# Optimization experiments

Hardware: AMD Instinct MI355X
Metric: run time of the kernel (lower is better)

The kernel has to match this reference:

```python
import jax, jax.numpy as jnp
import numpy as np

DIM = 1024
NUM_HEADS = 16
HEAD_DIM = DIM // NUM_HEADS
THETA = 10000.0


def apply_rope(x):
    # x: [B, S, H, D]; Llama-style interleaved rotary pairs.
    S, D = x.shape[1], x.shape[3]
    half = D // 2
    inv_freq = THETA ** (-jnp.arange(half, dtype=jnp.float32) * 2.0 / D)  # [D/2]
    angles = jnp.arange(S, dtype=jnp.float32)[:, None] * inv_freq[None, :]  # [S, D/2]
    cos = jnp.cos(angles)[None, :, None, :]  # [1,S,1,D/2]
    sin = jnp.sin(angles)[None, :, None, :]
    x_even = x[..., 0::2]
    x_odd = x[..., 1::2]
    out_even = x_even * cos - x_odd * sin
    out_odd = x_even * sin + x_odd * cos
    out = jnp.stack([out_even, out_odd], axis=-1).reshape(x.shape)
    return out.astype(x.dtype)


def setup_inputs() -> dict:
    key = jax.random.key(0)
    ks = jax.random.split(key, 5)
    B, S = 2, 2048
    x = jax.random.normal(ks[0], (B, S, DIM), dtype=jnp.float32)
    scale = 1.0 / np.sqrt(DIM)
    Wq = jax.random.normal(ks[1], (DIM, DIM), dtype=jnp.float32) * scale
    Wk = jax.random.normal(ks[2], (DIM, DIM), dtype=jnp.float32) * scale
    Wv = jax.random.normal(ks[3], (DIM, DIM), dtype=jnp.float32) * scale
    Wo = jax.random.normal(ks[4], (DIM, DIM), dtype=jnp.float32) * scale
    return {"x": x, "Wq": Wq, "Wk": Wk, "Wv": Wv, "Wo": Wo}


def reference(x, Wq, Wk, Wv, Wo):
    B, S, _ = x.shape
    # torch Linear: y = x @ W^T
    q = (x @ Wq.T).reshape(B, S, NUM_HEADS, HEAD_DIM)
    k = (x @ Wk.T).reshape(B, S, NUM_HEADS, HEAD_DIM)
    v = (x @ Wv.T).reshape(B, S, NUM_HEADS, HEAD_DIM)
    q = apply_rope(q)
    k = apply_rope(k)
    # causal SDPA, scale = 1/sqrt(head_dim)
    scale = 1.0 / np.sqrt(HEAD_DIM).astype(np.float32)
    scores = jnp.einsum("bqhd,bkhd->bhqk", q, k) * scale  # [B,H,S,S]
    causal = jnp.tril(jnp.ones((S, S), dtype=bool))
    scores = jnp.where(causal[None, None], scores, jnp.finfo(scores.dtype).min)
    attn = jax.nn.softmax(scores, axis=-1)
    y = jnp.einsum("bhqk,bkhd->bqhd", attn, v).reshape(B, S, DIM)
    return y @ Wo.T
```

## Files before the change

kernel.cpp:

```cpp
#include <hip/hip_runtime.h>
#include <hip/hip_bf16.h>

typedef __attribute__((ext_vector_type(8))) __bf16 bf16x8;
typedef __attribute__((ext_vector_type(4))) __bf16 bf16x4;
typedef __attribute__((ext_vector_type(4))) float f32x4;

#define DIM 1024
#define SLEN 2048
#define NH 16
#define HD 64

__device__ __forceinline__ f32x4 MFMA(bf16x8 a, bf16x8 b, f32x4 c) {
    return __builtin_amdgcn_mfma_f32_16x16x32_bf16(a, b, c, 0, 0, 0);
}

__global__ __launch_bounds__(256) void cvt_bf16(const float* __restrict__ in,
                                                __bf16* __restrict__ out, int n) {
    int i = (blockIdx.x * blockDim.x + threadIdx.x) * 8;
    if (i >= n) return;
    f32x4 a = *reinterpret_cast<const f32x4*>(in + i);
    f32x4 b = *reinterpret_cast<const f32x4*>(in + i + 4);
    bf16x8 o;
#pragma unroll
    for (int j = 0; j < 4; ++j) { o[j] = (__bf16)a[j]; o[j + 4] = (__bf16)b[j]; }
    *reinterpret_cast<bf16x8*>(out + i) = o;
}

__global__ __launch_bounds__(256) void cvt_w4(const float* __restrict__ w0,
                                              const float* __restrict__ w1,
                                              const float* __restrict__ w2,
                                              const float* __restrict__ w3,
                                              __bf16* __restrict__ o0,
                                              __bf16* __restrict__ o1,
                                              __bf16* __restrict__ o2,
                                              __bf16* __restrict__ o3) {
    int s = blockIdx.y;
    const float* in = s == 0 ? w0 : s == 1 ? w1 : s == 2 ? w2 : w3;
    __bf16* out = s == 0 ? o0 : s == 1 ? o1 : s == 2 ? o2 : o3;
    int i = (blockIdx.x * blockDim.x + threadIdx.x) * 8;
    f32x4 a = *reinterpret_cast<const f32x4*>(in + i);
    f32x4 b = *reinterpret_cast<const f32x4*>(in + i + 4);
    bf16x8 o;
#pragma unroll
    for (int j = 0; j < 4; ++j) { o[j] = (__bf16)a[j]; o[j + 4] = (__bf16)b[j]; }
    *reinterpret_cast<bf16x8*>(out + i) = o;
}

__global__ __launch_bounds__(256) void rope2(__bf16* __restrict__ q,
                                             __bf16* __restrict__ k) {
    __bf16* t = blockIdx.y == 0 ? q : k;
    const float scale = blockIdx.y == 0 ? 0.18033688011112042f : 1.0f;
    int idx = blockIdx.x * blockDim.x + threadIdx.x;
    int row = idx >> 9;
    int p = idx & 511;
    int head = p >> 5;
    int j = p & 31;
    int s = row & (SLEN - 1);
    float inv = expf(-0.28782313662425574f * (float)j);
    float angle = (float)s * inv;
    float sn, cs;
    sincosf(angle, &sn, &cs);
    size_t base = (size_t)row * DIM + head * HD + 2 * j;
    float e = (float)t[base], o = (float)t[base + 1];
    t[base] = (__bf16)((e * cs - o * sn) * scale);
    t[base + 1] = (__bf16)((e * sn + o * cs) * scale);
}

__global__ __launch_bounds__(256) void gemm_qkv(const __bf16* __restrict__ X,
                                                const __bf16* __restrict__ Wq,
                                                const __bf16* __restrict__ Wk,
                                                const __bf16* __restrict__ Wv,
                                                __bf16* __restrict__ Qo,
                                                __bf16* __restrict__ Ko,
                                                __bf16* __restrict__ Vt) {
    __shared__ alignas(16) __bf16 Alds[128 * 64];
    __shared__ alignas(16) __bf16 Blds[128 * 64];
    const int tid = threadIdx.x;
    const int lane = tid & 63;
    const int w = tid >> 6;
    const int wr = w >> 1, wc = w & 1;
    const int l15 = lane & 15, lhi = lane >> 4;
    const int l7 = l15 & 7;
    const int m0 = blockIdx.y * 128;
    const int n0g = blockIdx.x * 128;
    const int seg = n0g >> 10;
    const int n0 = n0g & 1023;
    const __bf16* __restrict__ B = seg == 0 ? Wq : seg == 1 ? Wk : Wv;
    const int K = 1024, N = 1024;

    const int lrow = lane >> 3;
    const int scol = ((lane & 7) ^ lrow) * 8;

    f32x4 acc[4][4] = {};

    for (int kt = 0; kt < K; kt += 64) {
#pragma unroll
        for (int c = 0; c < 4; ++c) {
            int r0 = c * 32 + w * 8;
            const __bf16* sa = &X[(size_t)(m0 + r0 + lrow) * K + kt + scol];
            const __bf16* sb = &B[(size_t)(n0 + r0 + lrow) * K + kt + scol];
            __builtin_amdgcn_global_load_lds((const __attribute__((address_space(1))) void*)sa,
                                             (__attribute__((address_space(3))) void*)&Alds[r0 * 64],
                                             16, 0, 0);
            __builtin_amdgcn_global_load_lds((const __attribute__((address_space(1))) void*)sb,
                                             (__attribute__((address_space(3))) void*)&Blds[r0 * 64],
                                             16, 0, 0);
        }
        __syncthreads();
#pragma unroll
        for (int kk = 0; kk < 2; ++kk) {
            bf16x8 af[4], bfr[4];
#pragma unroll
            for (int i = 0; i < 4; ++i) {
                af[i] = *(const bf16x8*)&Alds[(wr * 64 + i * 16 + l15) * 64 + 8 * ((kk * 4 + lhi) ^ l7)];
                bfr[i] = *(const bf16x8*)&Blds[(wc * 64 + i * 16 + l15) * 64 + 8 * ((kk * 4 + lhi) ^ l7)];
            }
            __builtin_amdgcn_s_setprio(1);
#pragma unroll
            for (int i = 0; i < 4; ++i)
#pragma unroll
                for (int j = 0; j < 4; ++j)
                    acc[i][j] = MFMA(af[i], bfr[j], acc[i][j]);
            __builtin_amdgcn_s_setprio(0);
        }
        __syncthreads();
    }
    if (seg < 2) {
        __bf16* __restrict__ O = seg == 0 ? Qo : Ko;
#pragma unroll
        for (int i = 0; i < 4; ++i)
#pragma unroll
            for (int j = 0; j < 4; ++j)
#pragma unroll
                for (int r = 0; r < 4; ++r) {
                    int row = m0 + wr * 64 + i * 16 + lhi * 4 + r;
                    int col = n0 + wc * 64 + j * 16 + l15;
                    O[(size_t)row * N + col] = (__bf16)acc[i][j][r];
                }
    } else {
#pragma unroll
        for (int i = 0; i < 4; ++i)
#pragma unroll
            for (int j = 0; j < 4; ++j) {
                int row = m0 + wr * 64 + i * 16 + lhi * 4;
                int col = n0 + wc * 64 + j * 16 + l15;
                int bb = row >> 11, s = row & 2047;
                int hh = col >> 6, d = col & 63;
                bf16x4 pk;
#pragma unroll
                for (int r = 0; r < 4; ++r) pk[r] = (__bf16)acc[i][j][r];
                *(bf16x4*)&Vt[((size_t)(bb * 16 + hh) * 64 + d) * SLEN + s] = pk;
            }
    }
}

__global__ __launch_bounds__(256) void gemm_o(const __bf16* __restrict__ A,
                                              const __bf16* __restrict__ B,
                                              float* __restrict__ C) {
    __shared__ alignas(16) __bf16 Alds[64 * 64];
    __shared__ alignas(16) __bf16 Blds[128 * 64];
    const int tid = threadIdx.x;
    const int lane = tid & 63;
    const int w = tid >> 6;
    const int wr = w >> 1, wc = w & 1;
    const int l15 = lane & 15, lhi = lane >> 4;
    const int l7 = l15 & 7;
    const int m0 = blockIdx.y * 64;
    const int n0 = blockIdx.x * 128;
    const int K = 1024, N = 1024;

    const int lrow = lane >> 3;
    const int scol = ((lane & 7) ^ lrow) * 8;

    f32x4 acc[2][4] = {};

    for (int kt = 0; kt < K; kt += 64) {
#pragma unroll
        for (int c = 0; c < 2; ++c) {
            int r0 = c * 32 + w * 8;
            const __bf16* sa = &A[(size_t)(m0 + r0 + lrow) * K + kt + scol];
            __builtin_amdgcn_global_load_lds((const __attribute__((address_space(1))) void*)sa,
                                             (__attribute__((address_space(3))) void*)&Alds[r0 * 64],
                                             16, 0, 0);
        }
#pragma unroll
        for (int c = 0; c < 4; ++c) {
            int r0 = c * 32 + w * 8;
            const __bf16* sb = &B[(size_t)(n0 + r0 + lrow) * K + kt + scol];
            __builtin_amdgcn_global_load_lds((const __attribute__((address_space(1))) void*)sb,
                                             (__attribute__((address_space(3))) void*)&Blds[r0 * 64],
                                             16, 0, 0);
        }
        __syncthreads();
#pragma unroll
        for (int kk = 0; kk < 2; ++kk) {
            bf16x8 af[2], bfr[4];
#pragma unroll
            for (int i = 0; i < 2; ++i)
                af[i] = *(const bf16x8*)&Alds[(wr * 32 + i * 16 + l15) * 64 + 8 * ((kk * 4 + lhi) ^ l7)];
#pragma unroll
            for (int j = 0; j < 4; ++j)
                bfr[j] = *(const bf16x8*)&Blds[(wc * 64 + j * 16 + l15) * 64 + 8 * ((kk * 4 + lhi) ^ l7)];
            __builtin_amdgcn_s_setprio(1);
#pragma unroll
            for (int i = 0; i < 2; ++i)
#pragma unroll
                for (int j = 0; j < 4; ++j)
                    acc[i][j] = MFMA(af[i], bfr[j], acc[i][j]);
            __builtin_amdgcn_s_setprio(0);
        }
        __syncthreads();
    }
#pragma unroll
    for (int i = 0; i < 2; ++i)
#pragma unroll
        for (int j = 0; j < 4; ++j)
#pragma unroll
            for (int r = 0; r < 4; ++r) {
                int row = m0 + wr * 32 + i * 16 + lhi * 4 + r;
                int col = n0 + wc * 64 + j * 16 + l15;
                C[(size_t)row * N + col] = acc[i][j][r];
            }
}

__global__ __launch_bounds__(256) void attn_kernel(const __bf16* __restrict__ Q,
                                                   const __bf16* __restrict__ K,
                                                   const __bf16* __restrict__ Vt,
                                                   __bf16* __restrict__ Y) {
    __shared__ __bf16 Klds[2][64 * 64];
    __shared__ __bf16 Vlds[2][64 * 64];
    __shared__ __bf16 Plds[4][16][68];

    const int tid = threadIdx.x;
    const int lane = tid & 63;
    const int w = tid >> 6;
    const int l15 = lane & 15, lhi = lane >> 4;
    const int l7 = l15 & 7;

    const int id = blockIdx.x;
    const int x = id & 7, j = id >> 3;
    const int qt = 31 - (j >> 2);
    const int bh = 4 * x + (j & 3);
    const int b = bh >> 4, h = bh & 15;

    const int srow = (lane >> 3);
    const int scs = (lane & 7) ^ srow;
    const __bf16* Kbase = K + (size_t)b * SLEN * DIM + h * HD;
    const __bf16* Vbase = Vt + (size_t)bh * 64 * SLEN;

    auto stage = [&](int buf, int kt) {
#pragma unroll
        for (int i = 0; i < 2; ++i) {
            int r0 = i * 32 + 8 * w + srow;
            const __bf16* sk = Kbase + (size_t)(kt * 64 + r0) * DIM + scs * 8;
            const __bf16* sv = Vbase + (size_t)r0 * SLEN + kt * 64 + scs * 8;
            __builtin_amdgcn_global_load_lds((const __attribute__((address_space(1))) void*)sk,
                                             (__attribute__((address_space(3))) void*)&Klds[buf][r0 * 64],
                                             16, 0, 0);
            __builtin_amdgcn_global_load_lds((const __attribute__((address_space(1))) void*)sv,
                                             (__attribute__((address_space(3))) void*)&Vlds[buf][r0 * 64],
                                             16, 0, 0);
        }
    };

    const int q0 = qt * 64;
    const int qrow_g = q0 + w * 16 + l15;
    const size_t qbase = (size_t)(b * SLEN + qrow_g) * DIM + h * HD;
    const bf16x8 qf0 = *(const bf16x8*)&Q[qbase + lhi * 8];
    const bf16x8 qf1 = *(const bf16x8*)&Q[qbase + 32 + lhi * 8];

    float m = -1e30f, lsum = 0.f;
    f32x4 acc[4] = {};

    const int nkt = qt + 1;
    stage(0, 0);
    for (int kt = 0; kt < nkt; ++kt) {
        const int cur = kt & 1;
        __syncthreads();
        if (kt + 1 < nkt) stage(cur ^ 1, kt + 1);

        f32x4 sT[4];
        __builtin_amdgcn_s_setprio(1);
#pragma unroll
        for (int nb = 0; nb < 4; ++nb) {
            const int krow = (nb * 16 + l15) * 64;
            bf16x8 k0 = *(const bf16x8*)&Klds[cur][krow + 8 * ((0 + lhi) ^ l7)];
            bf16x8 k1 = *(const bf16x8*)&Klds[cur][krow + 8 * ((4 + lhi) ^ l7)];
            f32x4 a = {};
            a = MFMA(k0, qf0, a);
            a = MFMA(k1, qf1, a);
            sT[nb] = a;
        }
        __builtin_amdgcn_s_setprio(0);
        if (kt == qt) {
#pragma unroll
            for (int nb = 0; nb < 4; ++nb)
#pragma unroll
                for (int r = 0; r < 4; ++r)
                    if (nb * 16 + lhi * 4 + r > w * 16 + l15) sT[nb][r] = -1e30f;
        }
        float mx = -1e30f;
#pragma unroll
        for (int nb = 0; nb < 4; ++nb)
#pragma unroll
            for (int r = 0; r < 4; ++r) mx = fmaxf(mx, sT[nb][r]);
        mx = fmaxf(mx, __shfl_xor(mx, 16));
        mx = fmaxf(mx, __shfl_xor(mx, 32));
        if (!__all(mx <= m + 8.0f)) {
            const float mnew = fmaxf(m, mx);
            const float corr = exp2f(m - mnew);
            m = mnew;
            lsum *= corr;
#pragma unroll
            for (int nd = 0; nd < 4; ++nd)
#pragma unroll
                for (int r = 0; r < 4; ++r) acc[nd][r] *= corr;
        }
        float rs = 0.f;
#pragma unroll
        for (int nb = 0; nb < 4; ++nb) {
            bf16x4 pk;
#pragma unroll
            for (int r = 0; r < 4; ++r) {
                float pv = exp2f(sT[nb][r] - m);
                rs += pv;
                pk[r] = (__bf16)pv;
            }
            *(bf16x4*)&Plds[w][l15][nb * 16 + lhi * 4] = pk;
        }
        rs += __shfl_xor(rs, 16);
        rs += __shfl_xor(rs, 32);
        lsum += rs;

        __builtin_amdgcn_s_setprio(1);
#pragma unroll
        for (int kk = 0; kk < 2; ++kk) {
            const bf16x8 pf = *(const bf16x8*)&Plds[w][l15][kk * 32 + lhi * 8];
#pragma unroll
            for (int nd = 0; nd < 4; ++nd) {
                const int vrow = (nd * 16 + l15) * 64;
                bf16x8 vf = *(const bf16x8*)&Vlds[cur][vrow + 8 * ((kk * 4 + lhi) ^ l7)];
                acc[nd] = MFMA(vf, pf, acc[nd]);
            }
        }
        __builtin_amdgcn_s_setprio(0);
    }
    const float inv = 1.0f / lsum;
#pragma unroll
    for (int nd = 0; nd < 4; ++nd) {
        bf16x4 o;
#pragma unroll
        for (int r = 0; r < 4; ++r) o[r] = (__bf16)(acc[nd][r] * inv);
        *(bf16x4*)&Y[(size_t)(b * SLEN + qrow_g) * DIM + h * HD + nd * 16 + lhi * 4] = o;
    }
}

extern "C" void kernel_launch(void* const* d_in, const int* in_sizes, int n_in,
                              void* d_out, int out_size, void* d_ws, size_t ws_size,
                              hipStream_t stream) {
    const float* x = (const float*)d_in[0];
    const float* Wq = (const float*)d_in[1];
    const float* Wk = (const float*)d_in[2];
    const float* Wv = (const float*)d_in[3];
    const float* Wo = (const float*)d_in[4];
    float* out = (float*)d_out;

    const size_t XN = (size_t)4096 * 1024;
    const size_t WN = (size_t)1024 * 1024;

    __bf16* xb = (__bf16*)d_ws;
    __bf16* qb = xb + XN;
    __bf16* kb = qb + XN;
    __bf16* vtb = kb + XN;
    __bf16* wqb = vtb + XN;
    __bf16* wkb = wqb + WN;
    __bf16* wvb = wkb + WN;
    __bf16* wob = wvb + WN;
    __bf16* yb = xb;

    cvt_bf16<<<XN / 8 / 256, 256, 0, stream>>>(x, xb, (int)XN);
    dim3 gw(WN / 8 / 256, 4);
    cvt_w4<<<gw, 256, 0, stream>>>(Wq, Wk, Wv, Wo, wqb, wkb, wvb, wob);

    dim3 gq(24, 32);
    gemm_qkv<<<gq, 256, 0, stream>>>(xb, wqb, wkb, wvb, qb, kb, vtb);

    int pairs = 4096 * (DIM / 2);
    dim3 gr(pairs / 256, 2);
    rope2<<<gr, 256, 0, stream>>>(qb, kb);

    attn_kernel<<<1024, 256, 0, stream>>>(qb, kb, vtb, yb);

    dim3 go(8, 64);
    gemm_o<<<go, 256, 0, stream>>>(yb, wob, out);
}
```

Baseline: 118.7 us.

## Fuse RoPE into QKV GEMM epilogue and compute softmax row sums via MFMA

Removes the separate rope2 kernel and applies the rotary embedding (plus the Q scale) inside the QKV GEMM epilogue, using a lane shuffle to fetch the paired even/odd element and fast __sincosf. In attention, the per-row softmax denominator is accumulated with an extra MFMA against a vector of ones instead of scalar adds and cross-lane shuffles. The P tile in LDS loses its padding and uses an XOR swizzle instead, and the row max uses a flatter reduction tree. This saves one kernel launch and a full read/write pass over Q and K, at the cost of lower-precision sincos and summing the denominator from bf16-rounded probabilities.

```diff
diff --git a/kernel.cpp b/kernel.cpp
--- a/kernel.cpp
+++ b/kernel.cpp
@@ -44,26 +44,6 @@
 #pragma unroll
     for (int j = 0; j < 4; ++j) { o[j] = (__bf16)a[j]; o[j + 4] = (__bf16)b[j]; }
     *reinterpret_cast<bf16x8*>(out + i) = o;
-}
-
-__global__ __launch_bounds__(256) void rope2(__bf16* __restrict__ q,
-                                             __bf16* __restrict__ k) {
-    __bf16* t = blockIdx.y == 0 ? q : k;
-    const float scale = blockIdx.y == 0 ? 0.18033688011112042f : 1.0f;
-    int idx = blockIdx.x * blockDim.x + threadIdx.x;
-    int row = idx >> 9;
-    int p = idx & 511;
-    int head = p >> 5;
-    int j = p & 31;
-    int s = row & (SLEN - 1);
-    float inv = expf(-0.28782313662425574f * (float)j);
-    float angle = (float)s * inv;
-    float sn, cs;
-    sincosf(angle, &sn, &cs);
-    size_t base = (size_t)row * DIM + head * HD + 2 * j;
-    float e = (float)t[base], o = (float)t[base + 1];
-    t[base] = (__bf16)((e * cs - o * sn) * scale);
-    t[base + 1] = (__bf16)((e * sn + o * cs) * scale);
 }
 
 __global__ __launch_bounds__(256) void gemm_qkv(const __bf16* __restrict__ X,
@@ -127,16 +107,27 @@
     }
     if (seg < 2) {
         __bf16* __restrict__ O = seg == 0 ? Qo : Ko;
-#pragma unroll
-        for (int i = 0; i < 4; ++i)
-#pragma unroll
-            for (int j = 0; j < 4; ++j)
+        const float qscale = seg == 0 ? 0.18033688011112042f : 1.0f;
+#pragma unroll
+        for (int j = 0; j < 4; ++j) {
+            const int col = n0 + wc * 64 + j * 16 + l15;
+            const int jp = (col & 63) >> 1;
+            const bool codd = col & 1;
+            const float invf = expf(-0.28782313662425574f * (float)jp);
+#pragma unroll
+            for (int i = 0; i < 4; ++i)
 #pragma unroll
                 for (int r = 0; r < 4; ++r) {
                     int row = m0 + wr * 64 + i * 16 + lhi * 4 + r;
-                    int col = n0 + wc * 64 + j * 16 + l15;
-                    O[(size_t)row * N + col] = (__bf16)acc[i][j][r];
+                    int s = row & (SLEN - 1);
+                    float sn, cs;
+                    __sincosf((float)s * invf, &sn, &cs);
+                    float own = acc[i][j][r];
+                    float oth = __shfl_xor(own, 1);
+                    float res = codd ? (oth * sn + own * cs) : (own * cs - oth * sn);
+                    O[(size_t)row * N + col] = (__bf16)(res * qscale);
                 }
+        }
     } else {
 #pragma unroll
         for (int i = 0; i < 4; ++i)
@@ -229,7 +220,7 @@
                                                    __bf16* __restrict__ Y) {
     __shared__ __bf16 Klds[2][64 * 64];
     __shared__ __bf16 Vlds[2][64 * 64];
-    __shared__ __bf16 Plds[4][16][68];
+    __shared__ __bf16 Plds[4][16][64];
 
     const int tid = threadIdx.x;
     const int lane = tid & 63;
@@ -269,8 +260,13 @@
     const bf16x8 qf0 = *(const bf16x8*)&Q[qbase + lhi * 8];
     const bf16x8 qf1 = *(const bf16x8*)&Q[qbase + 32 + lhi * 8];
 
-    float m = -1e30f, lsum = 0.f;
+    bf16x8 ones;
+#pragma unroll
+    for (int t = 0; t < 8; ++t) ones[t] = (__bf16)1.0f;
+
+    float m = -1e30f;
     f32x4 acc[4] = {};
+    f32x4 accL = {};
 
     const int nkt = qt + 1;
     stage(0, 0);
@@ -299,43 +295,45 @@
                 for (int r = 0; r < 4; ++r)
                     if (nb * 16 + lhi * 4 + r > w * 16 + l15) sT[nb][r] = -1e30f;
         }
-        float mx = -1e30f;
-#pragma unroll
-        for (int nb = 0; nb < 4; ++nb)
-#pragma unroll
-            for (int r = 0; r < 4; ++r) mx = fmaxf(mx, sT[nb][r]);
+        float t0 = fmaxf(fmaxf(sT[0][0], sT[0][1]), sT[0][2]);
+        float t1 = fmaxf(fmaxf(sT[0][3], sT[1][0]), sT[1][1]);
+        float t2 = fmaxf(fmaxf(sT[1][2], sT[1][3]), sT[2][0]);
+        float t3 = fmaxf(fmaxf(sT[2][1], sT[2][2]), sT[2][3]);
+        float t4 = fmaxf(fmaxf(sT[3][0], sT[3][1]), sT[3][2]);
+        float mx = fmaxf(fmaxf(fmaxf(t0, t1), fmaxf(t2, t3)), fmaxf(t4, sT[3][3]));
         mx = fmaxf(mx, __shfl_xor(mx, 16));
         mx = fmaxf(mx, __shfl_xor(mx, 32));
         if (!__all(mx <= m + 8.0f)) {
             const float mnew = fmaxf(m, mx);
             const float corr = exp2f(m - mnew);
             m = mnew;
-            lsum *= corr;
 #pragma unroll
             for (int nd = 0; nd < 4; ++nd)
 #pragma unroll
                 for (int r = 0; r < 4; ++r) acc[nd][r] *= corr;
-        }
-        float rs = 0.f;
+#pragma unroll
+            for (int r = 0; r < 4; ++r) accL[r] *= corr;
+        }
 #pragma unroll
         for (int nb = 0; nb < 4; ++nb) {
             bf16x4 pk;
 #pragma unroll
-            for (int r = 0; r < 4; ++r) {
-                float pv = exp2f(sT[nb][r] - m);
-                rs += pv;
-                pk[r] = (__bf16)pv;
-            }
-            *(bf16x4*)&Plds[w][l15][nb * 16 + lhi * 4] = pk;
-        }
-        rs += __shfl_xor(rs, 16);
-        rs += __shfl_xor(rs, 32);
-        lsum += rs;
+            for (int r = 0; r < 4; ++r) pk[r] = (__bf16)exp2f(sT[nb][r] - m);
+            const int cw = (nb * 4 + lhi) ^ l15;
+            *(bf16x4*)&Plds[w][l15][cw * 4] = pk;
+        }
 
         __builtin_amdgcn_s_setprio(1);
 #pragma unroll
         for (int kk = 0; kk < 2; ++kk) {
-            const bf16x8 pf = *(const bf16x8*)&Plds[w][l15][kk * 32 + lhi * 8];
+            const int c0 = (kk * 8 + lhi * 2) ^ l15;
+            const int c1 = c0 ^ 1;
+            bf16x4 plo = *(const bf16x4*)&Plds[w][l15][c0 * 4];
+            bf16x4 phi = *(const bf16x4*)&Plds[w][l15][c1 * 4];
+            bf16x8 pf;
+#pragma unroll
+            for (int t = 0; t < 4; ++t) { pf[t] = plo[t]; pf[t + 4] = phi[t]; }
+            accL = MFMA(ones, pf, accL);
 #pragma unroll
             for (int nd = 0; nd < 4; ++nd) {
                 const int vrow = (nd * 16 + l15) * 64;
@@ -345,7 +343,7 @@
         }
         __builtin_amdgcn_s_setprio(0);
     }
-    const float inv = 1.0f / lsum;
+    const float inv = 1.0f / accL[0];
 #pragma unroll
     for (int nd = 0; nd < 4; ++nd) {
         bf16x4 o;
@@ -385,10 +383,6 @@
     dim3 gq(24, 32);
     gemm_qkv<<<gq, 256, 0, stream>>>(xb, wqb, wkb, wvb, qb, kb, vtb);
 
-    int pairs = 4096 * (DIM / 2);
-    dim3 gr(pairs / 256, 2);
-    rope2<<<gr, 256, 0, stream>>>(qb, kb);
-
     attn_kernel<<<1024, 256, 0, stream>>>(qb, kb, vtb, yb);
 
     dim3 go(8, 64);
```

New measurement: 122.2 us. 1.03x slower.
